# Optimization experiments

Measured on AMD Instinct MI355X. Metric: run time of the kernel, lower is better.

Reference implementation:

```python
import jax, jax.numpy as jnp
import numpy as np

N_CELLS_RNA, N_GENES = 8000, 8000
N_CELLS_ATAC, N_REGIONS = 8000, 20000
N_FACTORS = 100

def setup_inputs() -> dict:
    key = jax.random.key(0)
    ks = jax.random.split(key, 10)
    return {
        "G": jax.random.uniform(ks[0], (N_CELLS_RNA, N_GENES), jnp.float32),
        "R": jax.random.uniform(ks[1], (N_CELLS_ATAC, N_REGIONS), jnp.float32),
        "A": jax.random.uniform(ks[2], (N_GENES, N_REGIONS), jnp.float32),
        "C_1": jax.random.uniform(ks[3], (N_CELLS_RNA, N_FACTORS), jnp.float32),
        "C_2": jax.random.uniform(ks[4], (N_CELLS_ATAC, N_FACTORS), jnp.float32),
        "C_g": jax.random.uniform(ks[5], (N_GENES, N_FACTORS), jnp.float32),
        "C_r": jax.random.uniform(ks[6], (N_REGIONS, N_FACTORS), jnp.float32),
        "A_g": jax.random.normal(ks[7], (N_FACTORS, N_FACTORS), jnp.float32),
        "A_r": jax.random.normal(ks[8], (N_FACTORS, N_FACTORS), jnp.float32),
        "b_g": jnp.zeros((1, N_GENES), jnp.float32),
        "b_r": jnp.zeros((1, N_REGIONS), jnp.float32),
        "b_1": jnp.zeros((N_CELLS_RNA, 1), jnp.float32),
        "b_2": jnp.zeros((N_CELLS_ATAC, 1), jnp.float32),
        "alpha": jnp.array([1000.0, 1000.0, 100.0, 10.0, 0.0], jnp.float32),
    }

def reference(G, R, A, C_1, C_2, C_g, C_r, A_g, A_r, b_g, b_r, b_1, b_2, alpha):
    sm = lambda X: jax.nn.softmax(X, axis=1)  # row-wise softmax as in torch dim=1
    S1, S2, Sg, Sr = sm(C_1), sm(C_2), sm(C_g), sm(C_r)
    # loss1: RNA reconstruction. [n1,N]@[N,N] then @[N,ng]
    rec_G = (S1 @ A_g) @ Sg.T
    loss1 = jnp.mean(jnp.square(G - rec_G - b_g - b_1))
    # loss2: ATAC reconstruction
    rec_R = (S2 @ A_r) @ Sr.T
    loss2 = jnp.mean(jnp.square(R - rec_R - b_r - b_2))
    # loss3: -trace(A_r^T A_g) / ||A_r|| / ||A_g||
    loss3 = -jnp.sum(A_r * A_g) / jnp.linalg.norm(A_r) / jnp.linalg.norm(A_g)
    # loss4: -trace(Sg^T (A Sr)) / ||Sg|| / ||A Sr||  (trace via elementwise sum)
    ASr = A @ Sr  # [ng, N]
    loss4 = -jnp.sum(Sg * ASr) / jnp.linalg.norm(Sg) / jnp.linalg.norm(ASr)
    l1 = alpha[0] * loss1
    l2 = alpha[1] * loss2
    l3 = alpha[2] * loss3
    l4 = alpha[3] * loss4
    loss = l1 + l2 + l3 + l4
    return jnp.stack([loss, l1, l2, l3, l4])
```

## Files before the change

### kernel.cpp

```cpp
#include <hip/hip_runtime.h>
#include <hip/hip_bf16.h>

typedef __bf16 bf16x8 __attribute__((ext_vector_type(8)));
typedef float  f32x4  __attribute__((ext_vector_type(4)));
typedef unsigned short us4 __attribute__((ext_vector_type(4)));
typedef unsigned short us8 __attribute__((ext_vector_type(8)));

#define N_CELLS 8000
#define N_GENES 8000
#define N_REG   20000
#define NF      100
#define KP      128
#define NFT     112
#define KSPLIT  25
#define NWIN    625

static __device__ __forceinline__ unsigned short f2bf_bits(float f) {
  unsigned u = __builtin_bit_cast(unsigned, f);
  u = (u + 0x7FFFu + ((u >> 16) & 1u)) >> 16;
  return (unsigned short)u;
}
static __device__ __forceinline__ float bf2f(unsigned short s) {
  unsigned u = ((unsigned)s) << 16;
  return __builtin_bit_cast(float, u);
}
static __device__ __forceinline__ bf16x8 cvt8n(f32x4 v0, f32x4 v1) {
  bf16x8 r;
  r[0] = __builtin_bit_cast(__bf16, __float2bfloat16(v0[0]));
  r[1] = __builtin_bit_cast(__bf16, __float2bfloat16(v0[1]));
  r[2] = __builtin_bit_cast(__bf16, __float2bfloat16(v0[2]));
  r[3] = __builtin_bit_cast(__bf16, __float2bfloat16(v0[3]));
  r[4] = __builtin_bit_cast(__bf16, __float2bfloat16(v1[0]));
  r[5] = __builtin_bit_cast(__bf16, __float2bfloat16(v1[1]));
  r[6] = __builtin_bit_cast(__bf16, __float2bfloat16(v1[2]));
  r[7] = __builtin_bit_cast(__bf16, __float2bfloat16(v1[3]));
  return r;
}

__global__ __launch_bounds__(256) void pre_kernel(
    const float* __restrict__ C1, const float* __restrict__ C2,
    const float* __restrict__ Cg, const float* __restrict__ Cr,
    const float* __restrict__ Ag, const float* __restrict__ Ar,
    unsigned short* __restrict__ T1, unsigned short* __restrict__ T2,
    unsigned short* __restrict__ Sg, unsigned short* __restrict__ Sr,
    float* __restrict__ accv) {
  __shared__ float srow[4][NF];
  int b = blockIdx.x, t = threadIdx.x;
  int w = t >> 6, lane = t & 63;
  if (b == 11000) {
    float d = 0.f, na = 0.f, nr = 0.f;
    for (int i = t; i < NF * NF; i += 256) {
      float a = Ag[i], r = Ar[i];
      d = fmaf(a, r, d); na = fmaf(a, a, na); nr = fmaf(r, r, nr);
    }
    #pragma unroll
    for (int off = 32; off > 0; off >>= 1) {
      d += __shfl_xor(d, off); na += __shfl_xor(na, off); nr += __shfl_xor(nr, off);
    }
    __shared__ float r3[3][4];
    if (lane == 0) { r3[0][w] = d; r3[1][w] = na; r3[2][w] = nr; }
    __syncthreads();
    if (t == 0) {
      accv[2] = r3[0][0] + r3[0][1] + r3[0][2] + r3[0][3];
      accv[3] = r3[1][0] + r3[1][1] + r3[1][2] + r3[1][3];
      accv[4] = r3[2][0] + r3[2][1] + r3[2][2] + r3[2][3];
    }
    return;
  }
  const float* C; const float* W = nullptr;
  unsigned short* outR = nullptr; unsigned short* outT = nullptr;
  int i;
  if (b < 2000)      { C = C1; W = Ag; outT = T1; i = b * 4 + w; }
  else if (b < 4000) { C = C2; W = Ar; outT = T2; i = (b - 2000) * 4 + w; }
  else if (b < 6000) { C = Cg; outR = Sg; i = (b - 4000) * 4 + w; }
  else               { C = Cr; outR = Sr; i = (b - 6000) * 4 + w; }

  float v0 = C[i * NF + lane];
  float v1 = (lane < 36) ? C[i * NF + 64 + lane] : -3.0e38f;
  float m = fmaxf(v0, v1);
  #pragma unroll
  for (int off = 32; off > 0; off >>= 1) m = fmaxf(m, __shfl_xor(m, off));
  float e0 = __expf(v0 - m);
  float e1 = (lane < 36) ? __expf(v1 - m) : 0.f;
  float s = e0 + e1;
  #pragma unroll
  for (int off = 32; off > 0; off >>= 1) s += __shfl_xor(s, off);
  float inv = 1.f / s;
  e0 *= inv; e1 *= inv;

  if (outT == nullptr) {
    outR[i * KP + lane] = f2bf_bits(e0);
    outR[i * KP + 64 + lane] = (lane < 36) ? f2bf_bits(e1) : (unsigned short)0;
    return;
  }
  srow[w][lane] = e0;
  if (lane < 36) srow[w][64 + lane] = e1;
  __syncthreads();
  int c2 = 64 + lane;
  int c2c = (c2 < NF) ? c2 : NF - 1;
  float a0=0.f, a1=0.f, a2=0.f, a3=0.f;
  float d0=0.f, d1=0.f, d2=0.f, d3=0.f;
  #pragma unroll 4
  for (int k = 0; k < NF; k += 4) {
    float s0 = srow[w][k], s1 = srow[w][k+1], s2 = srow[w][k+2], s3 = srow[w][k+3];
    a0 = fmaf(s0, W[(k  )*NF + lane], a0);
    a1 = fmaf(s1, W[(k+1)*NF + lane], a1);
    a2 = fmaf(s2, W[(k+2)*NF + lane], a2);
    a3 = fmaf(s3, W[(k+3)*NF + lane], a3);
    d0 = fmaf(s0, W[(k  )*NF + c2c], d0);
    d1 = fmaf(s1, W[(k+1)*NF + c2c], d1);
    d2 = fmaf(s2, W[(k+2)*NF + c2c], d2);
    d3 = fmaf(s3, W[(k+3)*NF + c2c], d3);
  }
  outT[i * KP + lane] = f2bf_bits((a0 + a1) + (a2 + a3));
  outT[i * KP + c2]   = (c2 < NF) ? f2bf_bits((d0 + d1) + (d2 + d3)) : (unsigned short)0;
}

__global__ __launch_bounds__(256) void bpack_kernel(
    const unsigned short* __restrict__ Sr,
    unsigned short* __restrict__ Bpack) {
  __shared__ unsigned short lds[64 * 128];
  int t = threadIdx.x;
  long r0 = (long)blockIdx.x * 64;
  int w0 = blockIdx.x * 2;
  int nv = (int)((N_REG - r0 < 64) ? (N_REG - r0) : 64);
  #pragma unroll
  for (int q = 0; q < 4; ++q) {
    int idx = q * 256 + t;
    int row = idx >> 4, col8 = (idx & 15) * 8;
    us8 v = {0, 0, 0, 0, 0, 0, 0, 0};
    if (row < nv) v = *reinterpret_cast<const us8*>(Sr + (r0 + row) * KP + col8);
    *reinterpret_cast<us8*>(lds + row * 128 + col8) = v;
  }
  __syncthreads();
  for (int idx = t; idx < 896; idx += 256) {
    int win = idx / 448, rem = idx - win * 448;
    int ni = rem >> 6, lane = rem & 63;
    int lr = lane & 15, lg = lane >> 4;
    if (w0 + win < NWIN) {
      us8 v;
      #pragma unroll
      for (int e = 0; e < 8; ++e)
        v[e] = lds[(win * 32 + lg * 8 + e) * 128 + ni * 16 + lr];
      *reinterpret_cast<us8*>(Bpack + (((long)(w0 + win) * 7 + ni) << 9) + (lane << 3)) = v;
    }
  }
}

__global__ __launch_bounds__(256, 3) void resid_kernel(
    const float* __restrict__ X,
    const unsigned short* __restrict__ Tm,
    const unsigned short* __restrict__ Sm,
    const float* __restrict__ bcol,
    const float* __restrict__ brow,
    int N, float* __restrict__ buckets) {
  __shared__ char ldsbuf[49152];
  char* ldsT = ldsbuf;
  char* ldsS = ldsbuf + 16384;
  int t = threadIdx.x;
  int wid = t >> 6, lane = t & 63;
  int lr = lane & 15, lg = lane >> 4;
  long r0blk = (long)blockIdx.y * 64;
  long c0blk = (long)blockIdx.x * 128;
  int r0 = (wid >> 1) * 32;
  int c0 = (wid & 1) * 64;

  bf16x8 sT[4], sS[8];
  #pragma unroll
  for (int i2 = 0; i2 < 4; ++i2) {
    int g = i2 * 256 + t, row = g >> 4, gi = g & 15;
    sT[i2] = *reinterpret_cast<const bf16x8*>(Tm + (r0blk + row) * KP + gi * 8);
  }
  #pragma unroll
  for (int i2 = 0; i2 < 8; ++i2) {
    int g = i2 * 256 + t, row = g >> 4, gi = g & 15;
    sS[i2] = *reinterpret_cast<const bf16x8*>(Sm + (c0blk + row) * KP + gi * 8);
  }

  f32x4 xv[2][4];
  #pragma unroll
  for (int ri = 0; ri < 2; ++ri) {
    long row = r0blk + r0 + ri * 16 + lr;
    #pragma unroll
    for (int ci = 0; ci < 4; ++ci) {
      long cb = c0blk + c0 + ci * 16 + lg * 4;
      if (cb < N) xv[ri][ci] = __builtin_nontemporal_load(
                    reinterpret_cast<const f32x4*>(X + row * N + cb));
      else        xv[ri][ci] = f32x4{0.f, 0.f, 0.f, 0.f};
    }
  }

  #pragma unroll
  for (int i2 = 0; i2 < 4; ++i2) {
    int g = i2 * 256 + t, row = g >> 4, gi = g & 15;
    int off = row * 256 + ((gi * 16) ^ ((row & 7) << 4));
    *reinterpret_cast<bf16x8*>(ldsT + off) = sT[i2];
  }
  #pragma unroll
  for (int i2 = 0; i2 < 8; ++i2) {
    int g = i2 * 256 + t, row = g >> 4, gi = g & 15;
    int off = row * 256 + ((gi * 16) ^ ((row & 7) << 4));
    *reinterpret_cast<bf16x8*>(ldsS + off) = sS[i2];
  }
  __syncthreads();

  f32x4 zero = {0.f, 0.f, 0.f, 0.f};
  f32x4 acc[4][2] = {{zero, zero}, {zero, zero}, {zero, zero}, {zero, zero}};
  #pragma unroll
  for (int ks = 0; ks < 4; ++ks) {
    bf16x8 a[4], bfr[2];
    #pragma unroll
    for (int ci = 0; ci < 4; ++ci) {
      int row = c0 + ci * 16 + lr;
      int off = row * 256 + (((ks * 64) + (lg * 16)) ^ ((row & 7) << 4));
      a[ci] = *reinterpret_cast<const bf16x8*>(ldsS + off);
    }
    #pragma unroll
    for (int ri = 0; ri < 2; ++ri) {
      int row = r0 + ri * 16 + lr;
      int off = row * 256 + (((ks * 64) + (lg * 16)) ^ ((row & 7) << 4));
      bfr[ri] = *reinterpret_cast<const bf16x8*>(ldsT + off);
    }
    #pragma unroll
    for (int ci = 0; ci < 4; ++ci)
      #pragma unroll
      for (int ri = 0; ri < 2; ++ri)
        acc[ci][ri] = __builtin_amdgcn_mfma_f32_16x16x32_bf16(a[ci], bfr[ri], acc[ci][ri], 0, 0, 0);
  }

  float brv[2];
  #pragma unroll
  for (int ri = 0; ri < 2; ++ri) brv[ri] = brow[r0blk + r0 + ri * 16 + lr];

  float sse = 0.f;
  #pragma unroll
  for (int ci = 0; ci < 4; ++ci) {
    long cb = c0blk + c0 + ci * 16 + lg * 4;
    if (cb < N) {
      f32x4 bc = *reinterpret_cast<const f32x4*>(bcol + cb);
      #pragma unroll
      for (int ri = 0; ri < 2; ++ri) {
        f32x4 x = xv[ri][ci];
        #pragma unroll
        for (int j = 0; j < 4; ++j) {
          float e = x[j] - acc[ci][ri][j] - bc[j] - brv[ri];
          sse = fmaf(e, e, sse);
        }
      }
    }
  }
  #pragma unroll
  for (int off = 32; off > 0; off >>= 1) sse += __shfl_xor(sse, off);
  __shared__ float wsum[4];
  if (lane == 0) wsum[wid] = sse;
  __syncthreads();
  if (t == 0)
    atomicAdd(&buckets[(blockIdx.y * gridDim.x + blockIdx.x) & 63],
              wsum[0] + wsum[1] + wsum[2] + wsum[3]);
}

__global__ __launch_bounds__(256, 4) void asr_kernel(
    const float* __restrict__ A,
    const unsigned short* __restrict__ Bpack,
    float* __restrict__ ASrN) {
  __shared__ char lds[2][16384];
  int t = threadIdx.x;
  int w = t >> 6, lane = t & 63;
  int lr = lane & 15, lg = lane >> 4;
  int gBase = blockIdx.x * 64;
  int kb0 = blockIdx.y * 800;
  int wk0 = blockIdx.y * 25;
  int ni0 = 2 * w;
  int ni1 = 2 * w + 1;
  bool has1 = (ni1 < 7);

  f32x4 zero = {0.f, 0.f, 0.f, 0.f};
  f32x4 acc[4][2];
  #pragma unroll
  for (int gt = 0; gt < 4; ++gt) { acc[gt][0] = zero; acc[gt][1] = zero; }
  f32x4 sreg[8];

  #pragma unroll
  for (int p = 0; p < 4; ++p) {
    int flat = p * 2048 + t * 8;
    int row = flat >> 7, kk = flat & 127;
    const float* src = A + (long)(gBase + row) * N_REG + kb0 + kk;
    sreg[2 * p]     = __builtin_nontemporal_load(reinterpret_cast<const f32x4*>(src));
    sreg[2 * p + 1] = __builtin_nontemporal_load(reinterpret_cast<const f32x4*>(src + 4));
  }

  #pragma unroll 1
  for (int it = 0; it < 7; ++it) {
    char* buf = lds[it & 1];
    if (it < 6) {
      #pragma unroll
      for (int p = 0; p < 4; ++p) {
        int flat = p * 2048 + t * 8;
        int row = flat >> 7, kk = flat & 127;
        int off = row * 256 + ((kk * 2) ^ ((row & 7) << 4));
        *reinterpret_cast<bf16x8*>(buf + off) = cvt8n(sreg[2 * p], sreg[2 * p + 1]);
      }
    } else {
      int row = t >> 2, kk = (t & 3) * 8;
      int off = row * 256 + ((kk * 2) ^ ((row & 7) << 4));
      *reinterpret_cast<bf16x8*>(buf + off) = cvt8n(sreg[0], sreg[1]);
    }
    __syncthreads();

    if (it < 5) {
      #pragma unroll
      for (int p = 0; p < 4; ++p) {
        int flat = p * 2048 + t * 8;
        int row = flat >> 7, kk = flat & 127;
        const float* src = A + (long)(gBase + row) * N_REG + kb0 + (it + 1) * 128 + kk;
        sreg[2 * p]     = __builtin_nontemporal_load(reinterpret_cast<const f32x4*>(src));
        sreg[2 * p + 1] = __builtin_nontemporal_load(reinterpret_cast<const f32x4*>(src + 4));
      }
    } else if (it == 5) {
      int row = t >> 2, kk = (t & 3) * 8;
      const float* src = A + (long)(gBase + row) * N_REG + kb0 + 768 + kk;
      sreg[0] = __builtin_nontemporal_load(reinterpret_cast<const f32x4*>(src));
      sreg[1] = __builtin_nontemporal_load(reinterpret_cast<const f32x4*>(src + 4));
    }

    int nk = (it < 6) ? 4 : 1;
    #pragma unroll 4
    for (int ks = 0; ks < nk; ++ks) {
      bf16x8 afr[4];
      #pragma unroll
      for (int gt = 0; gt < 4; ++gt) {
        int row = gt * 16 + lr;
        int off = row * 256 + (((ks * 64) + lg * 16) ^ ((row & 7) << 4));
        afr[gt] = *reinterpret_cast<const bf16x8*>(buf + off);
      }
      long wbase = ((long)(wk0 + it * 4 + ks) * 7) << 9;
      bf16x8 b0 = *reinterpret_cast<const bf16x8*>(
          Bpack + wbase + ((long)ni0 << 9) + (lane << 3));
      #pragma unroll
      for (int gt = 0; gt < 4; ++gt)
        acc[gt][0] = __builtin_amdgcn_mfma_f32_16x16x32_bf16(afr[gt], b0, acc[gt][0], 0, 0, 0);
      if (has1) {
        bf16x8 b1 = *reinterpret_cast<const bf16x8*>(
            Bpack + wbase + ((long)ni1 << 9) + (lane << 3));
        #pragma unroll
        for (int gt = 0; gt < 4; ++gt)
          acc[gt][1] = __builtin_amdgcn_mfma_f32_16x16x32_bf16(afr[gt], b1, acc[gt][1], 0, 0, 0);
      }
    }
  }

  float* slice = ASrN + (long)blockIdx.y * (N_GENES * NFT);
  #pragma unroll
  for (int gt = 0; gt < 4; ++gt) {
    int gb = gBase + gt * 16 + lg * 4;
    int f0 = ni0 * 16 + lr;
    #pragma unroll
    for (int j = 0; j < 4; ++j)
      __builtin_nontemporal_store(acc[gt][0][j], &slice[(gb + j) * NFT + f0]);
    if (has1) {
      int f1 = ni1 * 16 + lr;
      #pragma unroll
      for (int j = 0; j < 4; ++j)
        __builtin_nontemporal_store(acc[gt][1][j], &slice[(gb + j) * NFT + f1]);
    }
  }
}

__global__ void l4red_kernel(const unsigned short* __restrict__ Sgbf,
                             const float* __restrict__ ASrN,
                             float* __restrict__ accv) {
  const int NV = N_GENES * NFT / 4;
  int t = blockIdx.x * blockDim.x + threadIdx.x;
  float d = 0.f, n1 = 0.f, n2 = 0.f;
  for (int q = t; q < NV; q += gridDim.x * blockDim.x) {
    int g = q / (NFT / 4);
    int f4 = (q - g * (NFT / 4)) * 4;
    f32x4 av = {0.f, 0.f, 0.f, 0.f};
    #pragma unroll
    for (int s = 0; s < KSPLIT; ++s)
      av += __builtin_nontemporal_load(
              reinterpret_cast<const f32x4*>(ASrN + (long)s * (N_GENES * NFT) + g * NFT + f4));
    us4 sgb = *reinterpret_cast<const us4*>(Sgbf + g * KP + f4);
    #pragma unroll
    for (int j = 0; j < 4; ++j) {
      float sg = bf2f(sgb[j]);
      d = fmaf(sg, av[j], d); n1 = fmaf(sg, sg, n1); n2 = fmaf(av[j], av[j], n2);
    }
  }
  #pragma unroll
  for (int off = 32; off > 0; off >>= 1) {
    d += __shfl_xor(d, off); n1 += __shfl_xor(n1, off); n2 += __shfl_xor(n2, off);
  }
  __shared__ float r3[3][4];
  int lane = threadIdx.x & 63, w = threadIdx.x >> 6;
  if (lane == 0) { r3[0][w] = d; r3[1][w] = n1; r3[2][w] = n2; }
  __syncthreads();
  if (threadIdx.x == 0) {
    atomicAdd(&accv[5], r3[0][0] + r3[0][1] + r3[0][2] + r3[0][3]);
    atomicAdd(&accv[6], r3[1][0] + r3[1][1] + r3[1][2] + r3[1][3]);
    atomicAdd(&accv[7], r3[2][0] + r3[2][1] + r3[2][2] + r3[2][3]);
  }
}

__global__ void fin_kernel(const float* __restrict__ accv,
                           const float* __restrict__ bk1,
                           const float* __restrict__ bk2,
                           const float* __restrict__ alpha,
                           float* __restrict__ out) {
  if (threadIdx.x == 0) {
    float s1 = 0.f, s2 = 0.f;
    for (int i = 0; i < 64; ++i) { s1 += bk1[i]; s2 += bk2[i]; }
    float loss1 = s1 / 64000000.0f;
    float loss2 = s2 / 160000000.0f;
    float loss3 = -accv[2] / (sqrtf(accv[3]) * sqrtf(accv[4]));
    float loss4 = -accv[5] / (sqrtf(accv[6]) * sqrtf(accv[7]));
    float l1 = alpha[0] * loss1, l2 = alpha[1] * loss2;
    float l3 = alpha[2] * loss3, l4 = alpha[3] * loss4;
    out[0] = l1 + l2 + l3 + l4;
    out[1] = l1; out[2] = l2; out[3] = l3; out[4] = l4;
  }
}


extern "C" void kernel_launch(void* const* d_in, const int* in_sizes, int n_in,
                              void* d_out, int out_size, void* d_ws, size_t ws_size,
                              hipStream_t stream) {
  const float* G  = (const float*)d_in[0];
  const float* R  = (const float*)d_in[1];
  const float* A  = (const float*)d_in[2];
  const float* C1 = (const float*)d_in[3];
  const float* C2 = (const float*)d_in[4];
  const float* Cg = (const float*)d_in[5];
  const float* Cr = (const float*)d_in[6];
  const float* Ag = (const float*)d_in[7];
  const float* Ar = (const float*)d_in[8];
  const float* bg = (const float*)d_in[9];
  const float* br = (const float*)d_in[10];
  const float* b1 = (const float*)d_in[11];
  const float* b2 = (const float*)d_in[12];
  const float* alpha = (const float*)d_in[13];

  char* ws = (char*)d_ws;
  float* accv           = (float*)(ws + 0);
  float* buckets1       = (float*)(ws + 64);
  float* buckets2       = (float*)(ws + 320);
  float* ASrN           = (float*)(ws + 1024);
  unsigned short* T1    = (unsigned short*)(ws + 89601024);
  unsigned short* T2    = (unsigned short*)(ws + 91649024);
  unsigned short* Sg    = (unsigned short*)(ws + 93697024);
  unsigned short* Sr    = (unsigned short*)(ws + 95745024);
  unsigned short* Bpack = (unsigned short*)(ws + 100865024);

  hipMemsetAsync(d_ws, 0, 576, stream);

  pre_kernel<<<11001, 256, 0, stream>>>(C1, C2, Cg, Cr, Ag, Ar,
                                        T1, T2, Sg, Sr, accv);
  bpack_kernel<<<313, 256, 0, stream>>>(Sr, Bpack);

  resid_kernel<<<dim3(63, 125), 256, 0, stream>>>(G, T1, Sg, bg, b1, N_GENES, buckets1);
  resid_kernel<<<dim3(157, 125), 256, 0, stream>>>(R, T2, Sr, br, b2, N_REG, buckets2);

  asr_kernel<<<dim3(125, KSPLIT), 256, 0, stream>>>(A, Bpack, ASrN);

  l4red_kernel<<<128, 256, 0, stream>>>(Sg, ASrN, accv);
  fin_kernel<<<1, 64, 0, stream>>>(accv, buckets1, buckets2, alpha, (float*)d_out);
}
```

Before: 547.8 us.

## Store split-K ASr partials as bf16, double-buffer A prefetch registers

The split-K partial products of A@Sr are now written and read as bf16 instead of fp32, halving the intermediate traffic between asr_kernel and the reduction kernel. asr_kernel prefetches two tiles ahead using alternating register banks and drops to 3 waves/SIMD occupancy to make room for them. The reduction kernel gets a larger grid. Rounding each of the 25 partials to bf16 before summing adds error to the loss4 norms.

```diff
diff --git a/kernel.cpp b/kernel.cpp
--- a/kernel.cpp
+++ b/kernel.cpp
@@ -259,10 +259,10 @@
               wsum[0] + wsum[1] + wsum[2] + wsum[3]);
 }
 
-__global__ __launch_bounds__(256, 4) void asr_kernel(
+__global__ __launch_bounds__(256, 3) void asr_kernel(
     const float* __restrict__ A,
     const unsigned short* __restrict__ Bpack,
-    float* __restrict__ ASrN) {
+    unsigned short* __restrict__ ASrN) {
   __shared__ char lds[2][16384];
   int t = threadIdx.x;
   int w = t >> 6, lane = t & 63;
@@ -278,51 +278,56 @@
   f32x4 acc[4][2];
   #pragma unroll
   for (int gt = 0; gt < 4; ++gt) { acc[gt][0] = zero; acc[gt][1] = zero; }
-  f32x4 sreg[8];
-
+  f32x4 sregE[8], sregO[8];
+
+  int srow_[4], skk_[4];
   #pragma unroll
   for (int p = 0; p < 4; ++p) {
     int flat = p * 2048 + t * 8;
-    int row = flat >> 7, kk = flat & 127;
-    const float* src = A + (long)(gBase + row) * N_REG + kb0 + kk;
-    sreg[2 * p]     = __builtin_nontemporal_load(reinterpret_cast<const f32x4*>(src));
-    sreg[2 * p + 1] = __builtin_nontemporal_load(reinterpret_cast<const f32x4*>(src + 4));
+    srow_[p] = flat >> 7; skk_[p] = flat & 127;
+  }
+  int trow = t >> 2, tkk = (t & 3) * 8;
+
+  #pragma unroll
+  for (int p = 0; p < 4; ++p) {
+    const float* src = A + (long)(gBase + srow_[p]) * N_REG + kb0 + skk_[p];
+    sregE[2 * p]     = __builtin_nontemporal_load(reinterpret_cast<const f32x4*>(src));
+    sregE[2 * p + 1] = __builtin_nontemporal_load(reinterpret_cast<const f32x4*>(src + 4));
+  }
+  #pragma unroll
+  for (int p = 0; p < 4; ++p) {
+    const float* src = A + (long)(gBase + srow_[p]) * N_REG + kb0 + 128 + skk_[p];
+    sregO[2 * p]     = __builtin_nontemporal_load(reinterpret_cast<const f32x4*>(src));
+    sregO[2 * p + 1] = __builtin_nontemporal_load(reinterpret_cast<const f32x4*>(src + 4));
   }
 
   #pragma unroll 1
   for (int it = 0; it < 7; ++it) {
     char* buf = lds[it & 1];
+    f32x4* bank = (it & 1) ? sregO : sregE;
     if (it < 6) {
       #pragma unroll
       for (int p = 0; p < 4; ++p) {
-        int flat = p * 2048 + t * 8;
-        int row = flat >> 7, kk = flat & 127;
-        int off = row * 256 + ((kk * 2) ^ ((row & 7) << 4));
-        *reinterpret_cast<bf16x8*>(buf + off) = cvt8n(sreg[2 * p], sreg[2 * p + 1]);
+        int off = srow_[p] * 256 + ((skk_[p] * 2) ^ ((srow_[p] & 7) << 4));
+        *reinterpret_cast<bf16x8*>(buf + off) = cvt8n(bank[2 * p], bank[2 * p + 1]);
       }
     } else {
-      int row = t >> 2, kk = (t & 3) * 8;
-      int off = row * 256 + ((kk * 2) ^ ((row & 7) << 4));
-      *reinterpret_cast<bf16x8*>(buf + off) = cvt8n(sreg[0], sreg[1]);
+      int off = trow * 256 + ((tkk * 2) ^ ((trow & 7) << 4));
+      *reinterpret_cast<bf16x8*>(buf + off) = cvt8n(bank[0], bank[1]);
     }
     __syncthreads();
-
-    if (it < 5) {
+    if (it < 4) {
       #pragma unroll
       for (int p = 0; p < 4; ++p) {
-        int flat = p * 2048 + t * 8;
-        int row = flat >> 7, kk = flat & 127;
-        const float* src = A + (long)(gBase + row) * N_REG + kb0 + (it + 1) * 128 + kk;
-        sreg[2 * p]     = __builtin_nontemporal_load(reinterpret_cast<const f32x4*>(src));
-        sreg[2 * p + 1] = __builtin_nontemporal_load(reinterpret_cast<const f32x4*>(src + 4));
+        const float* src = A + (long)(gBase + srow_[p]) * N_REG + kb0 + (it + 2) * 128 + skk_[p];
+        bank[2 * p]     = __builtin_nontemporal_load(reinterpret_cast<const f32x4*>(src));
+        bank[2 * p + 1] = __builtin_nontemporal_load(reinterpret_cast<const f32x4*>(src + 4));
       }
-    } else if (it == 5) {
-      int row = t >> 2, kk = (t & 3) * 8;
-      const float* src = A + (long)(gBase + row) * N_REG + kb0 + 768 + kk;
-      sreg[0] = __builtin_nontemporal_load(reinterpret_cast<const f32x4*>(src));
-      sreg[1] = __builtin_nontemporal_load(reinterpret_cast<const f32x4*>(src + 4));
-    }
-
+    } else if (it == 4) {
+      const float* src = A + (long)(gBase + trow) * N_REG + kb0 + 768 + tkk;
+      bank[0] = __builtin_nontemporal_load(reinterpret_cast<const f32x4*>(src));
+      bank[1] = __builtin_nontemporal_load(reinterpret_cast<const f32x4*>(src + 4));
+    }
     int nk = (it < 6) ? 4 : 1;
     #pragma unroll 4
     for (int ks = 0; ks < nk; ++ks) {
@@ -349,25 +354,25 @@
     }
   }
 
-  float* slice = ASrN + (long)blockIdx.y * (N_GENES * NFT);
+  unsigned short* slice = ASrN + (long)blockIdx.y * (N_GENES * NFT);
   #pragma unroll
   for (int gt = 0; gt < 4; ++gt) {
     int gb = gBase + gt * 16 + lg * 4;
     int f0 = ni0 * 16 + lr;
     #pragma unroll
     for (int j = 0; j < 4; ++j)
-      __builtin_nontemporal_store(acc[gt][0][j], &slice[(gb + j) * NFT + f0]);
+      __builtin_nontemporal_store(f2bf_bits(acc[gt][0][j]), &slice[(gb + j) * NFT + f0]);
     if (has1) {
       int f1 = ni1 * 16 + lr;
       #pragma unroll
       for (int j = 0; j < 4; ++j)
-        __builtin_nontemporal_store(acc[gt][1][j], &slice[(gb + j) * NFT + f1]);
+        __builtin_nontemporal_store(f2bf_bits(acc[gt][1][j]), &slice[(gb + j) * NFT + f1]);
     }
   }
 }
 
 __global__ void l4red_kernel(const unsigned short* __restrict__ Sgbf,
-                             const float* __restrict__ ASrN,
+                             const unsigned short* __restrict__ ASrN,
                              float* __restrict__ accv) {
   const int NV = N_GENES * NFT / 4;
   int t = blockIdx.x * blockDim.x + threadIdx.x;
@@ -375,17 +380,18 @@
   for (int q = t; q < NV; q += gridDim.x * blockDim.x) {
     int g = q / (NFT / 4);
     int f4 = (q - g * (NFT / 4)) * 4;
-    f32x4 av = {0.f, 0.f, 0.f, 0.f};
-    #pragma unroll
-    for (int s = 0; s < KSPLIT; ++s)
-      av += __builtin_nontemporal_load(
-              reinterpret_cast<const f32x4*>(ASrN + (long)s * (N_GENES * NFT) + g * NFT + f4));
+    float av0 = 0.f, av1 = 0.f, av2 = 0.f, av3 = 0.f;
+    #pragma unroll
+    for (int s = 0; s < KSPLIT; ++s) {
+      us4 v = __builtin_nontemporal_load(
+          reinterpret_cast<const us4*>(ASrN + (long)s * (N_GENES * NFT) + g * NFT + f4));
+      av0 += bf2f(v[0]); av1 += bf2f(v[1]); av2 += bf2f(v[2]); av3 += bf2f(v[3]);
+    }
     us4 sgb = *reinterpret_cast<const us4*>(Sgbf + g * KP + f4);
-    #pragma unroll
-    for (int j = 0; j < 4; ++j) {
-      float sg = bf2f(sgb[j]);
-      d = fmaf(sg, av[j], d); n1 = fmaf(sg, sg, n1); n2 = fmaf(av[j], av[j], n2);
-    }
+    float sg0 = bf2f(sgb[0]), sg1 = bf2f(sgb[1]), sg2 = bf2f(sgb[2]), sg3 = bf2f(sgb[3]);
+    d = fmaf(sg0, av0, d); d = fmaf(sg1, av1, d); d = fmaf(sg2, av2, d); d = fmaf(sg3, av3, d);
+    n1 = fmaf(sg0, sg0, n1); n1 = fmaf(sg1, sg1, n1); n1 = fmaf(sg2, sg2, n1); n1 = fmaf(sg3, sg3, n1);
+    n2 = fmaf(av0, av0, n2); n2 = fmaf(av1, av1, n2); n2 = fmaf(av2, av2, n2); n2 = fmaf(av3, av3, n2);
   }
   #pragma unroll
   for (int off = 32; off > 0; off >>= 1) {
@@ -444,12 +450,12 @@
   float* accv           = (float*)(ws + 0);
   float* buckets1       = (float*)(ws + 64);
   float* buckets2       = (float*)(ws + 320);
-  float* ASrN           = (float*)(ws + 1024);
-  unsigned short* T1    = (unsigned short*)(ws + 89601024);
-  unsigned short* T2    = (unsigned short*)(ws + 91649024);
-  unsigned short* Sg    = (unsigned short*)(ws + 93697024);
-  unsigned short* Sr    = (unsigned short*)(ws + 95745024);
-  unsigned short* Bpack = (unsigned short*)(ws + 100865024);
+  unsigned short* ASrN  = (unsigned short*)(ws + 1024);
+  unsigned short* T1    = (unsigned short*)(ws + 44801024);
+  unsigned short* T2    = (unsigned short*)(ws + 46849024);
+  unsigned short* Sg    = (unsigned short*)(ws + 48897024);
+  unsigned short* Sr    = (unsigned short*)(ws + 50945024);
+  unsigned short* Bpack = (unsigned short*)(ws + 56065024);
 
   hipMemsetAsync(d_ws, 0, 576, stream);
 
@@ -462,6 +468,6 @@
 
   asr_kernel<<<dim3(125, KSPLIT), 256, 0, stream>>>(A, Bpack, ASrN);
 
-  l4red_kernel<<<128, 256, 0, stream>>>(Sg, ASrN, accv);
+  l4red_kernel<<<400, 256, 0, stream>>>(Sg, ASrN, accv);
   fin_kernel<<<1, 64, 0, stream>>>(accv, buckets1, buckets2, alpha, (float*)d_out);
 }
```

Measured after the change: 554.7 us. No clear change (+1.3%).

## Fuse residual and A@Sr kernels into one interleaved launch with bf16 partials

Applied to the files above, without the earlier changes.

Merges the two residual kernels and the A@Sr split-K kernel into a single launch whose blocks are proportionally interleaved, so that memory-bound residual work and the A-streaming GEMM can overlap and no tail or launch gap separates them. Split-K partials of A@Sr are now stored as bf16 instead of fp32, halving the partial buffer's write and read traffic. The final reduction is launched with more blocks. The cost is lower precision in the loss4 partial sums, and the A@Sr blocks now run under the residual kernel's occupancy bound and LDS size rather than their own.

```diff
diff --git a/kernel.cpp b/kernel.cpp
--- a/kernel.cpp
+++ b/kernel.cpp
@@ -14,6 +14,12 @@
 #define NFT     112
 #define KSPLIT  25
 #define NWIN    625
+
+#define NB_G   7875L
+#define NB_R   19625L
+#define NB_A   3125L
+#define NB_TOT 30625L
+#define NB_RA  22750L
 
 static __device__ __forceinline__ unsigned short f2bf_bits(float f) {
   unsigned u = __builtin_bit_cast(unsigned, f);
@@ -147,21 +153,23 @@
   }
 }
 
-__global__ __launch_bounds__(256, 3) void resid_kernel(
+static __device__ __forceinline__ void resid_body(
+    char* smem,
     const float* __restrict__ X,
     const unsigned short* __restrict__ Tm,
     const unsigned short* __restrict__ Sm,
     const float* __restrict__ bcol,
     const float* __restrict__ brow,
-    int N, float* __restrict__ buckets) {
-  __shared__ char ldsbuf[49152];
-  char* ldsT = ldsbuf;
-  char* ldsS = ldsbuf + 16384;
+    int N, float* __restrict__ buckets,
+    int bx, int by) {
+  char* ldsT = smem;
+  char* ldsS = smem + 16384;
+  float* wsum = (float*)(smem + 49152);
   int t = threadIdx.x;
   int wid = t >> 6, lane = t & 63;
   int lr = lane & 15, lg = lane >> 4;
-  long r0blk = (long)blockIdx.y * 64;
-  long c0blk = (long)blockIdx.x * 128;
+  long r0blk = (long)by * 64;
+  long c0blk = (long)bx * 128;
   int r0 = (wid >> 1) * 32;
   int c0 = (wid & 1) * 64;
 
@@ -251,25 +259,25 @@
   }
   #pragma unroll
   for (int off = 32; off > 0; off >>= 1) sse += __shfl_xor(sse, off);
-  __shared__ float wsum[4];
   if (lane == 0) wsum[wid] = sse;
   __syncthreads();
   if (t == 0)
-    atomicAdd(&buckets[(blockIdx.y * gridDim.x + blockIdx.x) & 63],
+    atomicAdd(&buckets[(by * 256 + bx) & 63],
               wsum[0] + wsum[1] + wsum[2] + wsum[3]);
 }
 
-__global__ __launch_bounds__(256, 4) void asr_kernel(
+static __device__ __forceinline__ void asr_body(
+    char* smem,
     const float* __restrict__ A,
     const unsigned short* __restrict__ Bpack,
-    float* __restrict__ ASrN) {
-  __shared__ char lds[2][16384];
+    unsigned short* __restrict__ ASrN,
+    int bx, int byk) {
   int t = threadIdx.x;
   int w = t >> 6, lane = t & 63;
   int lr = lane & 15, lg = lane >> 4;
-  int gBase = blockIdx.x * 64;
-  int kb0 = blockIdx.y * 800;
-  int wk0 = blockIdx.y * 25;
+  int gBase = bx * 64;
+  int kb0 = byk * 800;
+  int wk0 = byk * 25;
   int ni0 = 2 * w;
   int ni1 = 2 * w + 1;
   bool has1 = (ni1 < 7);
@@ -291,7 +299,7 @@
 
   #pragma unroll 1
   for (int it = 0; it < 7; ++it) {
-    char* buf = lds[it & 1];
+    char* buf = smem + (it & 1) * 16384;
     if (it < 6) {
       #pragma unroll
       for (int p = 0; p < 4; ++p) {
@@ -349,25 +357,57 @@
     }
   }
 
-  float* slice = ASrN + (long)blockIdx.y * (N_GENES * NFT);
+  unsigned short* slice = ASrN + (long)byk * (N_GENES * NFT);
   #pragma unroll
   for (int gt = 0; gt < 4; ++gt) {
     int gb = gBase + gt * 16 + lg * 4;
     int f0 = ni0 * 16 + lr;
     #pragma unroll
     for (int j = 0; j < 4; ++j)
-      __builtin_nontemporal_store(acc[gt][0][j], &slice[(gb + j) * NFT + f0]);
+      __builtin_nontemporal_store(f2bf_bits(acc[gt][0][j]), &slice[(gb + j) * NFT + f0]);
     if (has1) {
       int f1 = ni1 * 16 + lr;
       #pragma unroll
       for (int j = 0; j < 4; ++j)
-        __builtin_nontemporal_store(acc[gt][1][j], &slice[(gb + j) * NFT + f1]);
-    }
-  }
+        __builtin_nontemporal_store(f2bf_bits(acc[gt][1][j]), &slice[(gb + j) * NFT + f1]);
+    }
+  }
+}
+
+__global__ __launch_bounds__(256, 3) void mega_kernel(
+    const float* __restrict__ G, const float* __restrict__ R,
+    const float* __restrict__ A,
+    const unsigned short* __restrict__ T1, const unsigned short* __restrict__ T2,
+    const unsigned short* __restrict__ Sg, const unsigned short* __restrict__ Sr,
+    const unsigned short* __restrict__ Bpack,
+    const float* __restrict__ bg, const float* __restrict__ br,
+    const float* __restrict__ b1, const float* __restrict__ b2,
+    float* __restrict__ buckets1, float* __restrict__ buckets2,
+    unsigned short* __restrict__ ASrN) {
+  __shared__ char smem[49168];
+  long b = blockIdx.x;
+  long g_before = b * NB_G / NB_TOT;
+  long g_incl = (b + 1) * NB_G / NB_TOT;
+  if (g_incl > g_before) {
+    int idx = (int)g_before;
+    resid_body(smem, G, T1, Sg, bg, b1, N_GENES, buckets1, idx % 63, idx / 63);
+    return;
+  }
+  long j = b - g_before;
+  long a_before = j * NB_A / NB_RA;
+  long a_incl = (j + 1) * NB_A / NB_RA;
+  if (a_incl > a_before) {
+    int idx = (int)a_before;
+    asr_body(smem, A, Bpack, ASrN, idx % 125, idx / 125);
+    return;
+  }
+  long r = j - a_before;
+  int idx = (int)r;
+  resid_body(smem, R, T2, Sr, br, b2, N_REG, buckets2, idx % 157, idx / 157);
 }
 
 __global__ void l4red_kernel(const unsigned short* __restrict__ Sgbf,
-                             const float* __restrict__ ASrN,
+                             const unsigned short* __restrict__ ASrN,
                              float* __restrict__ accv) {
   const int NV = N_GENES * NFT / 4;
   int t = blockIdx.x * blockDim.x + threadIdx.x;
@@ -375,17 +415,18 @@
   for (int q = t; q < NV; q += gridDim.x * blockDim.x) {
     int g = q / (NFT / 4);
     int f4 = (q - g * (NFT / 4)) * 4;
-    f32x4 av = {0.f, 0.f, 0.f, 0.f};
-    #pragma unroll
-    for (int s = 0; s < KSPLIT; ++s)
-      av += __builtin_nontemporal_load(
-              reinterpret_cast<const f32x4*>(ASrN + (long)s * (N_GENES * NFT) + g * NFT + f4));
+    float av0 = 0.f, av1 = 0.f, av2 = 0.f, av3 = 0.f;
+    #pragma unroll
+    for (int s = 0; s < KSPLIT; ++s) {
+      us4 v = __builtin_nontemporal_load(
+          reinterpret_cast<const us4*>(ASrN + (long)s * (N_GENES * NFT) + g * NFT + f4));
+      av0 += bf2f(v[0]); av1 += bf2f(v[1]); av2 += bf2f(v[2]); av3 += bf2f(v[3]);
+    }
     us4 sgb = *reinterpret_cast<const us4*>(Sgbf + g * KP + f4);
-    #pragma unroll
-    for (int j = 0; j < 4; ++j) {
-      float sg = bf2f(sgb[j]);
-      d = fmaf(sg, av[j], d); n1 = fmaf(sg, sg, n1); n2 = fmaf(av[j], av[j], n2);
-    }
+    float sg0 = bf2f(sgb[0]), sg1 = bf2f(sgb[1]), sg2 = bf2f(sgb[2]), sg3 = bf2f(sgb[3]);
+    d = fmaf(sg0, av0, d); d = fmaf(sg1, av1, d); d = fmaf(sg2, av2, d); d = fmaf(sg3, av3, d);
+    n1 = fmaf(sg0, sg0, n1); n1 = fmaf(sg1, sg1, n1); n1 = fmaf(sg2, sg2, n1); n1 = fmaf(sg3, sg3, n1);
+    n2 = fmaf(av0, av0, n2); n2 = fmaf(av1, av1, n2); n2 = fmaf(av2, av2, n2); n2 = fmaf(av3, av3, n2);
   }
   #pragma unroll
   for (int off = 32; off > 0; off >>= 1) {
@@ -444,12 +485,12 @@
   float* accv           = (float*)(ws + 0);
   float* buckets1       = (float*)(ws + 64);
   float* buckets2       = (float*)(ws + 320);
-  float* ASrN           = (float*)(ws + 1024);
-  unsigned short* T1    = (unsigned short*)(ws + 89601024);
-  unsigned short* T2    = (unsigned short*)(ws + 91649024);
-  unsigned short* Sg    = (unsigned short*)(ws + 93697024);
-  unsigned short* Sr    = (unsigned short*)(ws + 95745024);
-  unsigned short* Bpack = (unsigned short*)(ws + 100865024);
+  unsigned short* ASrN  = (unsigned short*)(ws + 1024);
+  unsigned short* T1    = (unsigned short*)(ws + 44801024);
+  unsigned short* T2    = (unsigned short*)(ws + 46849024);
+  unsigned short* Sg    = (unsigned short*)(ws + 48897024);
+  unsigned short* Sr    = (unsigned short*)(ws + 50945024);
+  unsigned short* Bpack = (unsigned short*)(ws + 56065024);
 
   hipMemsetAsync(d_ws, 0, 576, stream);
 
@@ -457,11 +498,10 @@
                                         T1, T2, Sg, Sr, accv);
   bpack_kernel<<<313, 256, 0, stream>>>(Sr, Bpack);
 
-  resid_kernel<<<dim3(63, 125), 256, 0, stream>>>(G, T1, Sg, bg, b1, N_GENES, buckets1);
-  resid_kernel<<<dim3(157, 125), 256, 0, stream>>>(R, T2, Sr, br, b2, N_REG, buckets2);
-
-  asr_kernel<<<dim3(125, KSPLIT), 256, 0, stream>>>(A, Bpack, ASrN);
-
-  l4red_kernel<<<128, 256, 0, stream>>>(Sg, ASrN, accv);
+  mega_kernel<<<(int)NB_TOT, 256, 0, stream>>>(G, R, A, T1, T2, Sg, Sr, Bpack,
+                                               bg, br, b1, b2,
+                                               buckets1, buckets2, ASrN);
+
+  l4red_kernel<<<400, 256, 0, stream>>>(Sg, ASrN, accv);
   fin_kernel<<<1, 64, 0, stream>>>(accv, buckets1, buckets2, alpha, (float*)d_out);
 }
```

Result: slower. 559.5 us (+2.1%).
